# Performance work log

Hardware: AMD Instinct MI355X
Metric: run time of the kernel (lower is better)

Reference implementation:

```python
import math
import jax, jax.numpy as jnp
import numpy as np

DIM = 1024
DIM_HEAD = 64
NUM_HEAD = 16
HIDDEN = DIM_HEAD * NUM_HEAD  # 1024
B, L = 4, 2048
EPS = 1e-12  # torch F.normalize eps


def rms_norm(x, g):
    # F.normalize(x, dim=-1) * g * sqrt(d): L2-normalize then rescale
    d = x.shape[-1]
    norm = jnp.maximum(jnp.linalg.norm(x, axis=-1, keepdims=True), EPS)
    return x / norm * g * math.sqrt(d)


def setup_inputs() -> dict:
    key = jax.random.key(0)
    ks = jax.random.split(key, 8)
    x = jax.random.normal(ks[0], (B, L, DIM), dtype=jnp.float32)
    # torch Linear init scale ~ 1/sqrt(fan_in)
    s1 = 1.0 / math.sqrt(DIM)
    s2 = 1.0 / math.sqrt(HIDDEN)
    Wqkv = jax.random.uniform(ks[1], (3 * HIDDEN, DIM), minval=-s1, maxval=s1, dtype=jnp.float32)
    bqkv = jax.random.uniform(ks[2], (3 * HIDDEN,), minval=-s1, maxval=s1, dtype=jnp.float32)
    Wout = jax.random.uniform(ks[3], (DIM, HIDDEN), minval=-s2, maxval=s2, dtype=jnp.float32)
    bout = jax.random.uniform(ks[4], (DIM,), minval=-s2, maxval=s2, dtype=jnp.float32)
    g_q = jnp.ones((HIDDEN,), dtype=jnp.float32)
    g_k = jnp.ones((HIDDEN,), dtype=jnp.float32)
    g_out = jnp.ones((DIM,), dtype=jnp.float32)
    return {"x": x, "Wqkv": Wqkv, "bqkv": bqkv, "Wout": Wout, "bout": bout,
            "g_q": g_q, "g_k": g_k, "g_out": g_out}


def reference(x, Wqkv, bqkv, Wout, bout, g_q, g_k, g_out):
    scale = DIM_HEAD ** -0.5
    qkv = x @ Wqkv.T + bqkv  # (b, l, 3*hidden)
    q, k, v = jnp.split(qkv, 3, axis=-1)
    # QK RMSNorm applied over flattened (num_head*d) channel dim
    q = rms_norm(q, g_q)
    k = rms_norm(k, g_k)
    split_heads = lambda t: t.reshape(B, L, NUM_HEAD, DIM_HEAD).transpose(0, 2, 1, 3)
    q, k, v = split_heads(q), split_heads(k), split_heads(v)  # (b, h, l, d)
    q = q * scale
    sim = jnp.einsum('bhld,bhnd->bhln', q, k)
    attn = jax.nn.softmax(sim, axis=-1)
    out = jnp.einsum('bhln,bhnd->bhld', attn, v)  # (b, h, l, d)
    out = out.transpose(0, 2, 1, 3).reshape(B, L, HIDDEN)  # b l (h d)
    out = out @ Wout.T + bout
    return rms_norm(out, g_out)
```

## Files before the change

### kernel.cpp

```cpp
#include <hip/hip_runtime.h>
#include <math.h>

#define DIM       1024
#define DIM_HEAD  64
#define NUM_HEAD  16
#define HIDDEN    1024
#define BATCH     4
#define SEQ       2048
#define ROWS      (BATCH * SEQ)
#define QKV_N     (3 * HIDDEN)

typedef __bf16 bf16_t;
typedef __bf16 bf16x8 __attribute__((ext_vector_type(8)));
typedef __bf16 bf16x4 __attribute__((ext_vector_type(4)));
typedef float  f32x4  __attribute__((ext_vector_type(4)));

#define F32_ONE_PATTERN 0x3F800000u
#define LOG2E 1.44269504088896f

#define GLOAD_LDS16(gp, lp)                                                  \
    __builtin_amdgcn_global_load_lds(                                        \
        (const __attribute__((address_space(1))) void*)(const void*)(gp),    \
        (__attribute__((address_space(3))) void*)(void*)(lp), 16, 0, 0)

__global__ __launch_bounds__(256) void decode_bf16(const void* __restrict__ in,
                                                   bf16_t* __restrict__ out,
                                                   const unsigned* __restrict__ sniff,
                                                   long n)
{
    const bool isf32 = (*sniff == F32_ONE_PATTERN);
    const long i = ((long)blockIdx.x * 256 + threadIdx.x) * 8;
    if (i >= n) return;
    if (isf32) {
        const float* p = (const float*)in + i;
        f32x4 a = *(const f32x4*)p;
        f32x4 b = *(const f32x4*)(p + 4);
        bf16x8 r;
        r[0] = (bf16_t)a[0]; r[1] = (bf16_t)a[1]; r[2] = (bf16_t)a[2]; r[3] = (bf16_t)a[3];
        r[4] = (bf16_t)b[0]; r[5] = (bf16_t)b[1]; r[6] = (bf16_t)b[2]; r[7] = (bf16_t)b[3];
        *(bf16x8*)&out[i] = r;
    } else {
        *(bf16x8*)&out[i] = *(const bf16x8*)((const bf16_t*)in + i);
    }
}

__global__ __launch_bounds__(256) void decode_f32(const void* __restrict__ in,
                                                  float* __restrict__ out,
                                                  const unsigned* __restrict__ sniff,
                                                  long n)
{
    const bool isf32 = (*sniff == F32_ONE_PATTERN);
    const long i = ((long)blockIdx.x * 256 + threadIdx.x) * 8;
    if (i >= n) return;
    if (isf32) {
        const float* p = (const float*)in + i;
        *(f32x4*)&out[i]     = *(const f32x4*)p;
        *(f32x4*)&out[i + 4] = *(const f32x4*)(p + 4);
    } else {
        bf16x8 v = *(const bf16x8*)((const bf16_t*)in + i);
        f32x4 a, b;
        a[0] = (float)v[0]; a[1] = (float)v[1]; a[2] = (float)v[2]; a[3] = (float)v[3];
        b[0] = (float)v[4]; b[1] = (float)v[5]; b[2] = (float)v[6]; b[3] = (float)v[7];
        *(f32x4*)&out[i]     = a;
        *(f32x4*)&out[i + 4] = b;
    }
}

__global__ __launch_bounds__(256) void gemm_bt_bias(
    const bf16_t* __restrict__ A,
    const bf16_t* __restrict__ Bt,
    const float*  __restrict__ bias,
    bf16_t* __restrict__ C,
    int M, int N, int K)
{
    __shared__ __align__(16) bf16_t As[128 * 32];
    __shared__ __align__(16) bf16_t Bs[128 * 32];

    const int tid  = threadIdx.x;
    const int w    = tid >> 6;
    const int lane = tid & 63;
    const int wr   = w >> 1;
    const int wc   = w & 1;
    const int lr   = lane & 15;
    const int quad = lane >> 4;

    const int m0 = blockIdx.y * 128;
    const int n0 = blockIdx.x * 128;

    const int e0 = tid * 8;
    const int r0 = e0 >> 5;
    const int c0 = e0 & 31;
    const int r1 = r0 + 64;

    f32x4 acc[4][4];
    #pragma unroll
    for (int i = 0; i < 4; i++)
        #pragma unroll
        for (int j = 0; j < 4; j++)
            acc[i][j] = (f32x4){0.f, 0.f, 0.f, 0.f};

    const bf16_t* pa0 = &A [(size_t)(m0 + r0) * K + c0];
    const bf16_t* pa1 = &A [(size_t)(m0 + r1) * K + c0];
    const bf16_t* pb0 = &Bt[(size_t)(n0 + r0) * K + c0];
    const bf16_t* pb1 = &Bt[(size_t)(n0 + r1) * K + c0];

    for (int k0 = 0; k0 < K; k0 += 32) {
        __syncthreads();
        GLOAD_LDS16(pa0 + k0, &As[e0]);
        GLOAD_LDS16(pa1 + k0, &As[e0 + 2048]);
        GLOAD_LDS16(pb0 + k0, &Bs[e0]);
        GLOAD_LDS16(pb1 + k0, &Bs[e0 + 2048]);
        __syncthreads();

        bf16x8 af[4], bfr[4];
        #pragma unroll
        for (int i = 0; i < 4; i++)
            af[i] = *(const bf16x8*)&As[(wr * 64 + i * 16 + lr) * 32 + quad * 8];
        #pragma unroll
        for (int j = 0; j < 4; j++)
            bfr[j] = *(const bf16x8*)&Bs[(wc * 64 + j * 16 + lr) * 32 + quad * 8];
        #pragma unroll
        for (int i = 0; i < 4; i++)
            #pragma unroll
            for (int j = 0; j < 4; j++)
                acc[i][j] = __builtin_amdgcn_mfma_f32_16x16x32_bf16(
                    af[i], bfr[j], acc[i][j], 0, 0, 0);
    }

    #pragma unroll
    for (int i = 0; i < 4; i++) {
        const int row = m0 + wr * 64 + i * 16 + quad * 4;
        #pragma unroll
        for (int j = 0; j < 4; j++) {
            const int col = n0 + wc * 64 + j * 16 + lr;
            const float bv = bias[col];
            f32x4 v = acc[i][j];
            #pragma unroll
            for (int r = 0; r < 4; r++)
                C[(size_t)(row + r) * N + col] = (bf16_t)(v[r] + bv);
        }
    }
}

__device__ __forceinline__ void norm_apply(bf16_t* __restrict__ row,
                                           const float* __restrict__ g,
                                           float mult, int tid, float* red)
{
    bf16x4 xv = *(const bf16x4*)&row[tid * 4];
    float f0 = (float)xv[0], f1 = (float)xv[1], f2 = (float)xv[2], f3 = (float)xv[3];
    float ss = f0 * f0 + f1 * f1 + f2 * f2 + f3 * f3;
    #pragma unroll
    for (int off = 32; off > 0; off >>= 1) ss += __shfl_xor(ss, off, 64);
    if ((tid & 63) == 0) red[tid >> 6] = ss;
    __syncthreads();
    const float tot  = red[0] + red[1] + red[2] + red[3];
    const float fac  = mult / fmaxf(sqrtf(tot), 1e-12f);
    f32x4 gv = *(const f32x4*)&g[tid * 4];
    bf16x4 o;
    o[0] = (bf16_t)(f0 * gv[0] * fac);
    o[1] = (bf16_t)(f1 * gv[1] * fac);
    o[2] = (bf16_t)(f2 * gv[2] * fac);
    o[3] = (bf16_t)(f3 * gv[3] * fac);
    *(bf16x4*)&row[tid * 4] = o;
    __syncthreads();
}

__global__ __launch_bounds__(256) void qk_rmsnorm(bf16_t* __restrict__ qkv,
                                                  const float* __restrict__ gq,
                                                  const float* __restrict__ gk)
{
    __shared__ float red[4];
    const size_t base = (size_t)blockIdx.x * QKV_N;
    norm_apply(qkv + base, gq, 4.0f * LOG2E, threadIdx.x, red);
    norm_apply(qkv + base + HIDDEN, gk, 32.0f, threadIdx.x, red);
}

__global__ __launch_bounds__(256) void final_rmsnorm(const bf16_t* __restrict__ in,
                                                     const float* __restrict__ g,
                                                     void* __restrict__ out,
                                                     const unsigned* __restrict__ sniff)
{
    __shared__ float red[4];
    const bool isf32 = (*sniff == F32_ONE_PATTERN);
    const int tid = threadIdx.x;
    const bf16_t* row = in + (size_t)blockIdx.x * HIDDEN;

    bf16x4 xv = *(const bf16x4*)&row[tid * 4];
    float f0 = (float)xv[0], f1 = (float)xv[1], f2 = (float)xv[2], f3 = (float)xv[3];
    float ss = f0 * f0 + f1 * f1 + f2 * f2 + f3 * f3;
    #pragma unroll
    for (int off = 32; off > 0; off >>= 1) ss += __shfl_xor(ss, off, 64);
    if ((tid & 63) == 0) red[tid >> 6] = ss;
    __syncthreads();
    const float tot = red[0] + red[1] + red[2] + red[3];
    const float fac = 32.0f / fmaxf(sqrtf(tot), 1e-12f);
    f32x4 gv = *(const f32x4*)&g[tid * 4];
    f32x4 o;
    o[0] = f0 * gv[0] * fac;
    o[1] = f1 * gv[1] * fac;
    o[2] = f2 * gv[2] * fac;
    o[3] = f3 * gv[3] * fac;
    if (isf32) {
        *(f32x4*)((float*)out + (size_t)blockIdx.x * HIDDEN + tid * 4) = o;
    } else {
        bf16x4 ob;
        ob[0] = (bf16_t)o[0]; ob[1] = (bf16_t)o[1];
        ob[2] = (bf16_t)o[2]; ob[3] = (bf16_t)o[3];
        *(bf16x4*)((bf16_t*)out + (size_t)blockIdx.x * HIDDEN + tid * 4) = ob;
    }
}

__global__ __launch_bounds__(256) void transpose_v(const bf16_t* __restrict__ qkv,
                                                   bf16_t* __restrict__ vt)
{
    __shared__ bf16_t t[64][72];
    const int tid = threadIdx.x;
    const int bh = blockIdx.y, b = bh >> 4, h = bh & 15;
    const int l0 = blockIdx.x * 64;
    #pragma unroll
    for (int i = 0; i < 2; i++) {
        const int u = tid + i * 256;
        const int row = u >> 3, cg = u & 7;
        *(bf16x8*)&t[row][cg * 8] =
            *(const bf16x8*)&qkv[(size_t)(b * SEQ + l0 + row) * QKV_N + 2 * HIDDEN + h * 64 + cg * 8];
    }
    __syncthreads();
    #pragma unroll
    for (int i = 0; i < 2; i++) {
        const int u = tid + i * 256;
        const int d = u >> 3, lg = u & 7;
        bf16x8 o;
        #pragma unroll
        for (int e = 0; e < 8; e++) o[e] = t[lg * 8 + e][d];
        *(bf16x8*)&vt[((size_t)bh * 64 + d) * SEQ + l0 + lg * 8] = o;
    }
}

__global__ __launch_bounds__(256) void attn_mfma4(const bf16_t* __restrict__ qkv,
                                                  const bf16_t* __restrict__ vt,
                                                  bf16_t* __restrict__ out)
{
    __shared__ __align__(16) union {
        bf16_t Ps[4][64 * 40];
        float  Obuf[2][64][68];
    } sh;
    __shared__ float lred[4][4][16];

    const int tid  = threadIdx.x;
    const int w    = tid >> 6;
    const int lane = tid & 63;
    const int l15  = lane & 15;
    const int quad = lane >> 4;

    const int j    = blockIdx.x;
    const int xcd  = j & 7;
    const int slot = j >> 3;
    const int bh   = ((slot >> 5) << 3) | xcd;
    const int q0   = (slot & 31) * 64;
    const int b = bh >> 4, h = bh & 15;

    bf16x8 qf[4][2];
    #pragma unroll
    for (int qt = 0; qt < 4; qt++) {
        const bf16_t* qrow = qkv + (size_t)(b * SEQ + q0 + qt * 16 + l15) * QKV_N + h * DIM_HEAD;
        qf[qt][0] = *(const bf16x8*)&qrow[quad * 8];
        qf[qt][1] = *(const bf16x8*)&qrow[32 + quad * 8];
    }

    f32x4 O[4][4];
    float lp[4] = {0.f, 0.f, 0.f, 0.f};
    #pragma unroll
    for (int qt = 0; qt < 4; qt++)
        #pragma unroll
        for (int dt = 0; dt < 4; dt++)
            O[qt][dt] = (f32x4){0.f, 0.f, 0.f, 0.f};

    const bf16_t* kptr = qkv + (size_t)(b * SEQ + w * 32) * QKV_N + HIDDEN + h * DIM_HEAD;
    const bf16_t* vptr = vt + (size_t)bh * 64 * SEQ + w * 32;
    const int koff0 = l15 * QKV_N + quad * 8;
    const int koff1 = (16 + l15) * QKV_N + quad * 8;
    const int voff  = l15 * SEQ + quad * 8;
    bf16_t* const psw = sh.Ps[w] + l15 * 40 + quad * 4;
    const bf16_t* const psr = sh.Ps[w] + l15 * 40 + quad * 8;

    for (int it = 0; it < SEQ / 128; it++) {
        bf16x8 kA[2][2], vB[4];
        kA[0][0] = *(const bf16x8*)(kptr + koff0);
        kA[0][1] = *(const bf16x8*)(kptr + koff0 + 32);
        kA[1][0] = *(const bf16x8*)(kptr + koff1);
        kA[1][1] = *(const bf16x8*)(kptr + koff1 + 32);
        #pragma unroll
        for (int dt = 0; dt < 4; dt++)
            vB[dt] = *(const bf16x8*)(vptr + voff + dt * 16 * SEQ);
        kptr += 128 * QKV_N;
        vptr += 128;

        f32x4 s[2][4];
        #pragma unroll
        for (int kt = 0; kt < 2; kt++)
            #pragma unroll
            for (int qt = 0; qt < 4; qt++) {
                f32x4 z = (f32x4){0.f, 0.f, 0.f, 0.f};
                z = __builtin_amdgcn_mfma_f32_16x16x32_bf16(kA[kt][0], qf[qt][0], z, 0, 0, 0);
                s[kt][qt] = __builtin_amdgcn_mfma_f32_16x16x32_bf16(kA[kt][1], qf[qt][1], z, 0, 0, 0);
            }

        #pragma unroll
        for (int qt = 0; qt < 4; qt++)
            #pragma unroll
            for (int kt = 0; kt < 2; kt++) {
                bf16x4 pk;
                #pragma unroll
                for (int r = 0; r < 4; r++) {
                    const float p = __builtin_amdgcn_exp2f(s[kt][qt][r]);
                    lp[qt] += p;
                    pk[r] = (bf16_t)p;
                }
                *(bf16x4*)(psw + qt * 640 + kt * 16) = pk;
            }
        __builtin_amdgcn_s_waitcnt(0xC07F);

        #pragma unroll
        for (int qt = 0; qt < 4; qt++) {
            bf16x8 pf = *(const bf16x8*)(psr + qt * 640);
            #pragma unroll
            for (int dt = 0; dt < 4; dt++)
                O[qt][dt] = __builtin_amdgcn_mfma_f32_16x16x32_bf16(pf, vB[dt], O[qt][dt], 0, 0, 0);
        }
    }

    #pragma unroll
    for (int qt = 0; qt < 4; qt++) {
        lp[qt] += __shfl_xor(lp[qt], 16, 64);
        lp[qt] += __shfl_xor(lp[qt], 32, 64);
    }
    __syncthreads();
    if (w >= 2) {
        #pragma unroll
        for (int qt = 0; qt < 4; qt++)
            #pragma unroll
            for (int dt = 0; dt < 4; dt++)
                #pragma unroll
                for (int r = 0; r < 4; r++)
                    sh.Obuf[w - 2][qt * 16 + quad * 4 + r][dt * 16 + l15] = O[qt][dt][r];
    }
    if (quad == 0) {
        #pragma unroll
        for (int qt = 0; qt < 4; qt++) lred[w][qt][l15] = lp[qt];
    }
    __syncthreads();
    if (w < 2) {
        #pragma unroll
        for (int qt = 0; qt < 4; qt++)
            #pragma unroll
            for (int dt = 0; dt < 4; dt++)
                #pragma unroll
                for (int r = 0; r < 4; r++) {
                    float* p = &sh.Obuf[w][qt * 16 + quad * 4 + r][dt * 16 + l15];
                    *p += O[qt][dt][r];
                }
    }
    __syncthreads();
    #pragma unroll
    for (int i = 0; i < 2; i++) {
        const int u   = tid + i * 256;
        const int row = u >> 3;
        const int c8  = (u & 7) * 8;
        const float ls = lred[0][row >> 4][row & 15] + lred[1][row >> 4][row & 15]
                       + lred[2][row >> 4][row & 15] + lred[3][row >> 4][row & 15];
        const float inv = 1.0f / ls;
        f32x4 a0 = *(const f32x4*)&sh.Obuf[0][row][c8];
        f32x4 a1 = *(const f32x4*)&sh.Obuf[0][row][c8 + 4];
        f32x4 b0 = *(const f32x4*)&sh.Obuf[1][row][c8];
        f32x4 b1 = *(const f32x4*)&sh.Obuf[1][row][c8 + 4];
        bf16x8 o;
        o[0] = (bf16_t)((a0[0] + b0[0]) * inv);
        o[1] = (bf16_t)((a0[1] + b0[1]) * inv);
        o[2] = (bf16_t)((a0[2] + b0[2]) * inv);
        o[3] = (bf16_t)((a0[3] + b0[3]) * inv);
        o[4] = (bf16_t)((a1[0] + b1[0]) * inv);
        o[5] = (bf16_t)((a1[1] + b1[1]) * inv);
        o[6] = (bf16_t)((a1[2] + b1[2]) * inv);
        o[7] = (bf16_t)((a1[3] + b1[3]) * inv);
        *(bf16x8*)&out[(size_t)(b * SEQ + q0 + row) * HIDDEN + h * DIM_HEAD + c8] = o;
    }
}

extern "C" void kernel_launch(void* const* d_in, const int* in_sizes, int n_in,
                              void* d_out, int out_size, void* d_ws, size_t ws_size,
                              hipStream_t stream)
{
    (void)in_sizes; (void)n_in; (void)out_size; (void)ws_size;
    const void* x_raw    = d_in[0];
    const void* Wqkv_raw = d_in[1];
    const void* bqkv_raw = d_in[2];
    const void* Wout_raw = d_in[3];
    const void* bout_raw = d_in[4];
    const void* gq_raw   = d_in[5];
    const void* gk_raw   = d_in[6];
    const void* gout_raw = d_in[7];
    const unsigned* sniff = (const unsigned*)d_in[5];

    char* ws = (char*)d_ws;
    bf16_t* xb      = (bf16_t*)(ws + 0);
    bf16_t* Wqkvb   = (bf16_t*)(ws + (16l << 20));
    bf16_t* Woutb   = (bf16_t*)(ws + (22l << 20));
    float*  bqkv_f  = (float*) (ws + (24l << 20));
    float*  bout_f  = (float*) (ws + (24l << 20) + 16384);
    float*  gq_f    = (float*) (ws + (24l << 20) + 2 * 16384);
    float*  gk_f    = (float*) (ws + (24l << 20) + 3 * 16384);
    float*  gout_f  = (float*) (ws + (24l << 20) + 4 * 16384);
    bf16_t* qkv     = (bf16_t*)(ws + (25l << 20));
    bf16_t* vtb     = (bf16_t*)(ws + (73l << 20));
    bf16_t* attn_o  = xb;
    bf16_t* out_b   = qkv;

    decode_bf16<<<(ROWS * DIM) / 2048, 256, 0, stream>>>(x_raw, xb, sniff, (long)ROWS * DIM);
    decode_bf16<<<(QKV_N * DIM) / 2048, 256, 0, stream>>>(Wqkv_raw, Wqkvb, sniff, (long)QKV_N * DIM);
    decode_bf16<<<(DIM * HIDDEN) / 2048, 256, 0, stream>>>(Wout_raw, Woutb, sniff, (long)DIM * HIDDEN);
    decode_f32<<<2, 256, 0, stream>>>(bqkv_raw, bqkv_f, sniff, QKV_N);
    decode_f32<<<1, 256, 0, stream>>>(bout_raw, bout_f, sniff, DIM);
    decode_f32<<<1, 256, 0, stream>>>(gq_raw, gq_f, sniff, HIDDEN);
    decode_f32<<<1, 256, 0, stream>>>(gk_raw, gk_f, sniff, HIDDEN);
    decode_f32<<<1, 256, 0, stream>>>(gout_raw, gout_f, sniff, DIM);

    gemm_bt_bias<<<dim3(QKV_N / 128, ROWS / 128), 256, 0, stream>>>(
        xb, Wqkvb, bqkv_f, qkv, ROWS, QKV_N, DIM);
    qk_rmsnorm<<<ROWS, 256, 0, stream>>>(qkv, gq_f, gk_f);
    transpose_v<<<dim3(SEQ / 64, BATCH * NUM_HEAD), 256, 0, stream>>>(qkv, vtb);
    attn_mfma4<<<(SEQ / 64) * BATCH * NUM_HEAD, 256, 0, stream>>>(qkv, vtb, attn_o);
    gemm_bt_bias<<<dim3(HIDDEN / 128, ROWS / 128), 256, 0, stream>>>(
        attn_o, Woutb, bout_f, out_b, ROWS, HIDDEN, DIM);
    final_rmsnorm<<<ROWS, 256, 0, stream>>>(out_b, gout_f, d_out, sniff);
}
```

Baseline: 372.5 us.

## Halve attention query tile, compute row sums via MFMA, merge param decodes

The attention kernel now handles 32 query rows per block instead of 64, doubling the grid and cutting per-wave registers, with launch bounds requesting 4 blocks per CU. Softmax denominators are computed by an extra MFMA against a ones vector rather than scalar adds plus cross-lane shuffles, and the sums are stored in a spare shared-memory column. The five small parameter-decode launches are merged into one. The trade-off is that K/V tiles are reloaded twice as often per query and each iteration issues an extra MFMA.

Result: slower. 469.3 us (+26.0%).

```diff
diff --git a/kernel.cpp b/kernel.cpp
--- a/kernel.cpp
+++ b/kernel.cpp
@@ -44,25 +44,31 @@
     }
 }
 
-__global__ __launch_bounds__(256) void decode_f32(const void* __restrict__ in,
-                                                  float* __restrict__ out,
-                                                  const unsigned* __restrict__ sniff,
-                                                  long n)
+__global__ __launch_bounds__(256) void decode_params(
+    const void* __restrict__ bqkv_raw, const void* __restrict__ bout_raw,
+    const void* __restrict__ gq_raw,   const void* __restrict__ gk_raw,
+    const void* __restrict__ gout_raw,
+    float* __restrict__ o_bqkv, float* __restrict__ o_bout,
+    float* __restrict__ o_gq,   float* __restrict__ o_gk,
+    float* __restrict__ o_gout,
+    const unsigned* __restrict__ sniff)
 {
     const bool isf32 = (*sniff == F32_ONE_PATTERN);
-    const long i = ((long)blockIdx.x * 256 + threadIdx.x) * 8;
-    if (i >= n) return;
+    const int blk = blockIdx.x;
+    const void* src; float* dst; int off;
+    if (blk < 3)       { src = bqkv_raw; dst = o_bqkv; off = blk * 1024; }
+    else if (blk == 3) { src = bout_raw; dst = o_bout; off = 0; }
+    else if (blk == 4) { src = gq_raw;   dst = o_gq;   off = 0; }
+    else if (blk == 5) { src = gk_raw;   dst = o_gk;   off = 0; }
+    else               { src = gout_raw; dst = o_gout; off = 0; }
+    const int i = off + threadIdx.x * 4;
     if (isf32) {
-        const float* p = (const float*)in + i;
-        *(f32x4*)&out[i]     = *(const f32x4*)p;
-        *(f32x4*)&out[i + 4] = *(const f32x4*)(p + 4);
+        *(f32x4*)&dst[i] = *((const f32x4*)src + (off >> 2) + threadIdx.x);
     } else {
-        bf16x8 v = *(const bf16x8*)((const bf16_t*)in + i);
-        f32x4 a, b;
+        bf16x4 v = *((const bf16x4*)src + (off >> 2) + threadIdx.x);
+        f32x4 a;
         a[0] = (float)v[0]; a[1] = (float)v[1]; a[2] = (float)v[2]; a[3] = (float)v[3];
-        b[0] = (float)v[4]; b[1] = (float)v[5]; b[2] = (float)v[6]; b[3] = (float)v[7];
-        *(f32x4*)&out[i]     = a;
-        *(f32x4*)&out[i + 4] = b;
+        *(f32x4*)&dst[i] = a;
     }
 }
 
@@ -236,15 +242,14 @@
     }
 }
 
-__global__ __launch_bounds__(256) void attn_mfma4(const bf16_t* __restrict__ qkv,
-                                                  const bf16_t* __restrict__ vt,
-                                                  bf16_t* __restrict__ out)
+__global__ __launch_bounds__(256, 4) void attn_mfma5(const bf16_t* __restrict__ qkv,
+                                                     const bf16_t* __restrict__ vt,
+                                                     bf16_t* __restrict__ out)
 {
     __shared__ __align__(16) union {
-        bf16_t Ps[4][64 * 40];
-        float  Obuf[2][64][68];
+        bf16_t Ps[4][32 * 40];
+        float  Obuf[2][32][68];
     } sh;
-    __shared__ float lred[4][4][16];
 
     const int tid  = threadIdx.x;
     const int w    = tid >> 6;
@@ -255,25 +260,31 @@
     const int j    = blockIdx.x;
     const int xcd  = j & 7;
     const int slot = j >> 3;
-    const int bh   = ((slot >> 5) << 3) | xcd;
-    const int q0   = (slot & 31) * 64;
+    const int bh   = ((slot >> 6) << 3) | xcd;
+    const int q0   = (slot & 63) * 32;
     const int b = bh >> 4, h = bh & 15;
 
-    bf16x8 qf[4][2];
-    #pragma unroll
-    for (int qt = 0; qt < 4; qt++) {
+    bf16x8 qf[2][2];
+    #pragma unroll
+    for (int qt = 0; qt < 2; qt++) {
         const bf16_t* qrow = qkv + (size_t)(b * SEQ + q0 + qt * 16 + l15) * QKV_N + h * DIM_HEAD;
         qf[qt][0] = *(const bf16x8*)&qrow[quad * 8];
         qf[qt][1] = *(const bf16x8*)&qrow[32 + quad * 8];
     }
 
-    f32x4 O[4][4];
-    float lp[4] = {0.f, 0.f, 0.f, 0.f};
-    #pragma unroll
-    for (int qt = 0; qt < 4; qt++)
+    f32x4 O[2][4];
+    f32x4 ls[2];
+    #pragma unroll
+    for (int qt = 0; qt < 2; qt++) {
+        ls[qt] = (f32x4){0.f, 0.f, 0.f, 0.f};
         #pragma unroll
         for (int dt = 0; dt < 4; dt++)
             O[qt][dt] = (f32x4){0.f, 0.f, 0.f, 0.f};
+    }
+    bf16x8 vones;
+    #pragma unroll
+    for (int e = 0; e < 8; e++) vones[e] = (bf16_t)1.0f;
+    const f32x4 fzero = (f32x4){0.f, 0.f, 0.f, 0.f};
 
     const bf16_t* kptr = qkv + (size_t)(b * SEQ + w * 32) * QKV_N + HIDDEN + h * DIM_HEAD;
     const bf16_t* vptr = vt + (size_t)bh * 64 * SEQ + w * 32;
@@ -295,80 +306,73 @@
         kptr += 128 * QKV_N;
         vptr += 128;
 
-        f32x4 s[2][4];
+        f32x4 s[2][2];
         #pragma unroll
         for (int kt = 0; kt < 2; kt++)
             #pragma unroll
-            for (int qt = 0; qt < 4; qt++) {
-                f32x4 z = (f32x4){0.f, 0.f, 0.f, 0.f};
-                z = __builtin_amdgcn_mfma_f32_16x16x32_bf16(kA[kt][0], qf[qt][0], z, 0, 0, 0);
+            for (int qt = 0; qt < 2; qt++) {
+                f32x4 z = __builtin_amdgcn_mfma_f32_16x16x32_bf16(kA[kt][0], qf[qt][0], fzero, 0, 0, 0);
                 s[kt][qt] = __builtin_amdgcn_mfma_f32_16x16x32_bf16(kA[kt][1], qf[qt][1], z, 0, 0, 0);
             }
 
         #pragma unroll
-        for (int qt = 0; qt < 4; qt++)
+        for (int qt = 0; qt < 2; qt++)
             #pragma unroll
             for (int kt = 0; kt < 2; kt++) {
                 bf16x4 pk;
                 #pragma unroll
-                for (int r = 0; r < 4; r++) {
-                    const float p = __builtin_amdgcn_exp2f(s[kt][qt][r]);
-                    lp[qt] += p;
-                    pk[r] = (bf16_t)p;
-                }
+                for (int r = 0; r < 4; r++)
+                    pk[r] = (bf16_t)__builtin_amdgcn_exp2f(s[kt][qt][r]);
                 *(bf16x4*)(psw + qt * 640 + kt * 16) = pk;
             }
         __builtin_amdgcn_s_waitcnt(0xC07F);
 
         #pragma unroll
-        for (int qt = 0; qt < 4; qt++) {
+        for (int qt = 0; qt < 2; qt++) {
             bf16x8 pf = *(const bf16x8*)(psr + qt * 640);
+            ls[qt] = __builtin_amdgcn_mfma_f32_16x16x32_bf16(pf, vones, ls[qt], 0, 0, 0);
             #pragma unroll
             for (int dt = 0; dt < 4; dt++)
                 O[qt][dt] = __builtin_amdgcn_mfma_f32_16x16x32_bf16(pf, vB[dt], O[qt][dt], 0, 0, 0);
         }
     }
 
-    #pragma unroll
-    for (int qt = 0; qt < 4; qt++) {
-        lp[qt] += __shfl_xor(lp[qt], 16, 64);
-        lp[qt] += __shfl_xor(lp[qt], 32, 64);
-    }
     __syncthreads();
     if (w >= 2) {
         #pragma unroll
-        for (int qt = 0; qt < 4; qt++)
+        for (int qt = 0; qt < 2; qt++) {
             #pragma unroll
             for (int dt = 0; dt < 4; dt++)
                 #pragma unroll
                 for (int r = 0; r < 4; r++)
                     sh.Obuf[w - 2][qt * 16 + quad * 4 + r][dt * 16 + l15] = O[qt][dt][r];
-    }
-    if (quad == 0) {
-        #pragma unroll
-        for (int qt = 0; qt < 4; qt++) lred[w][qt][l15] = lp[qt];
+            if (l15 == 0)
+                #pragma unroll
+                for (int r = 0; r < 4; r++)
+                    sh.Obuf[w - 2][qt * 16 + quad * 4 + r][64] = ls[qt][r];
+        }
     }
     __syncthreads();
     if (w < 2) {
         #pragma unroll
-        for (int qt = 0; qt < 4; qt++)
+        for (int qt = 0; qt < 2; qt++) {
             #pragma unroll
             for (int dt = 0; dt < 4; dt++)
                 #pragma unroll
-                for (int r = 0; r < 4; r++) {
-                    float* p = &sh.Obuf[w][qt * 16 + quad * 4 + r][dt * 16 + l15];
-                    *p += O[qt][dt][r];
-                }
-    }
-    __syncthreads();
-    #pragma unroll
-    for (int i = 0; i < 2; i++) {
-        const int u   = tid + i * 256;
+                for (int r = 0; r < 4; r++)
+                    sh.Obuf[w][qt * 16 + quad * 4 + r][dt * 16 + l15] += O[qt][dt][r];
+            if (l15 == 0)
+                #pragma unroll
+                for (int r = 0; r < 4; r++)
+                    sh.Obuf[w][qt * 16 + quad * 4 + r][64] += ls[qt][r];
+        }
+    }
+    __syncthreads();
+    {
+        const int u   = tid;
         const int row = u >> 3;
         const int c8  = (u & 7) * 8;
-        const float ls = lred[0][row >> 4][row & 15] + lred[1][row >> 4][row & 15]
-                       + lred[2][row >> 4][row & 15] + lred[3][row >> 4][row & 15];
-        const float inv = 1.0f / ls;
+        const float inv = 1.0f / (sh.Obuf[0][row][64] + sh.Obuf[1][row][64]);
         f32x4 a0 = *(const f32x4*)&sh.Obuf[0][row][c8];
         f32x4 a1 = *(const f32x4*)&sh.Obuf[0][row][c8 + 4];
         f32x4 b0 = *(const f32x4*)&sh.Obuf[1][row][c8];
@@ -418,17 +422,14 @@
     decode_bf16<<<(ROWS * DIM) / 2048, 256, 0, stream>>>(x_raw, xb, sniff, (long)ROWS * DIM);
     decode_bf16<<<(QKV_N * DIM) / 2048, 256, 0, stream>>>(Wqkv_raw, Wqkvb, sniff, (long)QKV_N * DIM);
     decode_bf16<<<(DIM * HIDDEN) / 2048, 256, 0, stream>>>(Wout_raw, Woutb, sniff, (long)DIM * HIDDEN);
-    decode_f32<<<2, 256, 0, stream>>>(bqkv_raw, bqkv_f, sniff, QKV_N);
-    decode_f32<<<1, 256, 0, stream>>>(bout_raw, bout_f, sniff, DIM);
-    decode_f32<<<1, 256, 0, stream>>>(gq_raw, gq_f, sniff, HIDDEN);
-    decode_f32<<<1, 256, 0, stream>>>(gk_raw, gk_f, sniff, HIDDEN);
-    decode_f32<<<1, 256, 0, stream>>>(gout_raw, gout_f, sniff, DIM);
+    decode_params<<<7, 256, 0, stream>>>(bqkv_raw, bout_raw, gq_raw, gk_raw, gout_raw,
+                                         bqkv_f, bout_f, gq_f, gk_f, gout_f, sniff);
 
     gemm_bt_bias<<<dim3(QKV_N / 128, ROWS / 128), 256, 0, stream>>>(
         xb, Wqkvb, bqkv_f, qkv, ROWS, QKV_N, DIM);
     qk_rmsnorm<<<ROWS, 256, 0, stream>>>(qkv, gq_f, gk_f);
     transpose_v<<<dim3(SEQ / 64, BATCH * NUM_HEAD), 256, 0, stream>>>(qkv, vtb);
-    attn_mfma4<<<(SEQ / 64) * BATCH * NUM_HEAD, 256, 0, stream>>>(qkv, vtb, attn_o);
+    attn_mfma5<<<(SEQ / 32) * BATCH * NUM_HEAD, 256, 0, stream>>>(qkv, vtb, attn_o);
     gemm_bt_bias<<<dim3(HIDDEN / 128, ROWS / 128), 256, 0, stream>>>(
         attn_o, Woutb, bout_f, out_b, ROWS, HIDDEN, DIM);
     final_rmsnorm<<<ROWS, 256, 0, stream>>>(out_b, gout_f, d_out, sniff);
```

## Fuse V transpose into QKV GEMM epilogue and merge param decode launches

Applied to the files above, without the earlier changes.

The QKV GEMM is split so that Q/K columns go to a compact row-major buffer while V columns are written transposed straight into the per-head V^T layout. This removes the separate transpose_v kernel and its extra read and write of V. The five small parameter-decode launches are merged into one 7-block kernel to cut launch overhead. The transposed epilogue writes 4-element strided stores, which may coalesce worse than the old row-major store.

Result: faster. 356.4 us (-4.3%).

```diff
diff --git a/kernel.cpp b/kernel.cpp
--- a/kernel.cpp
+++ b/kernel.cpp
@@ -9,6 +9,7 @@
 #define SEQ       2048
 #define ROWS      (BATCH * SEQ)
 #define QKV_N     (3 * HIDDEN)
+#define QK_N      2048
 
 typedef __bf16 bf16_t;
 typedef __bf16 bf16x8 __attribute__((ext_vector_type(8)));
@@ -44,34 +45,40 @@
     }
 }
 
-__global__ __launch_bounds__(256) void decode_f32(const void* __restrict__ in,
-                                                  float* __restrict__ out,
-                                                  const unsigned* __restrict__ sniff,
-                                                  long n)
+__global__ __launch_bounds__(256) void decode_params(
+    const void* __restrict__ bqkv_raw, const void* __restrict__ bout_raw,
+    const void* __restrict__ gq_raw,   const void* __restrict__ gk_raw,
+    const void* __restrict__ gout_raw,
+    float* __restrict__ o_bqkv, float* __restrict__ o_bout,
+    float* __restrict__ o_gq,   float* __restrict__ o_gk,
+    float* __restrict__ o_gout,
+    const unsigned* __restrict__ sniff)
 {
     const bool isf32 = (*sniff == F32_ONE_PATTERN);
-    const long i = ((long)blockIdx.x * 256 + threadIdx.x) * 8;
-    if (i >= n) return;
+    const int blk = blockIdx.x;
+    const void* src; float* dst; int off;
+    if (blk < 3)       { src = bqkv_raw; dst = o_bqkv; off = blk * 1024; }
+    else if (blk == 3) { src = bout_raw; dst = o_bout; off = 0; }
+    else if (blk == 4) { src = gq_raw;   dst = o_gq;   off = 0; }
+    else if (blk == 5) { src = gk_raw;   dst = o_gk;   off = 0; }
+    else               { src = gout_raw; dst = o_gout; off = 0; }
+    const int i = off + threadIdx.x * 4;
     if (isf32) {
-        const float* p = (const float*)in + i;
-        *(f32x4*)&out[i]     = *(const f32x4*)p;
-        *(f32x4*)&out[i + 4] = *(const f32x4*)(p + 4);
+        *(f32x4*)&dst[i] = *((const f32x4*)src + (off >> 2) + threadIdx.x);
     } else {
-        bf16x8 v = *(const bf16x8*)((const bf16_t*)in + i);
-        f32x4 a, b;
+        bf16x4 v = *((const bf16x4*)src + (off >> 2) + threadIdx.x);
+        f32x4 a;
         a[0] = (float)v[0]; a[1] = (float)v[1]; a[2] = (float)v[2]; a[3] = (float)v[3];
-        b[0] = (float)v[4]; b[1] = (float)v[5]; b[2] = (float)v[6]; b[3] = (float)v[7];
-        *(f32x4*)&out[i]     = a;
-        *(f32x4*)&out[i + 4] = b;
-    }
-}
-
-__global__ __launch_bounds__(256) void gemm_bt_bias(
+        *(f32x4*)&dst[i] = a;
+    }
+}
+
+__global__ __launch_bounds__(256) void gemm_qkv(
     const bf16_t* __restrict__ A,
     const bf16_t* __restrict__ Bt,
     const float*  __restrict__ bias,
-    bf16_t* __restrict__ C,
-    int M, int N, int K)
+    bf16_t* __restrict__ qk,
+    bf16_t* __restrict__ vt)
 {
     __shared__ __align__(16) bf16_t As[128 * 32];
     __shared__ __align__(16) bf16_t Bs[128 * 32];
@@ -86,6 +93,106 @@
 
     const int m0 = blockIdx.y * 128;
     const int n0 = blockIdx.x * 128;
+    const int K  = DIM;
+
+    const int e0 = tid * 8;
+    const int r0 = e0 >> 5;
+    const int c0 = e0 & 31;
+    const int r1 = r0 + 64;
+
+    f32x4 acc[4][4];
+    #pragma unroll
+    for (int i = 0; i < 4; i++)
+        #pragma unroll
+        for (int j = 0; j < 4; j++)
+            acc[i][j] = (f32x4){0.f, 0.f, 0.f, 0.f};
+
+    const bf16_t* pa0 = &A [(size_t)(m0 + r0) * K + c0];
+    const bf16_t* pa1 = &A [(size_t)(m0 + r1) * K + c0];
+    const bf16_t* pb0 = &Bt[(size_t)(n0 + r0) * K + c0];
+    const bf16_t* pb1 = &Bt[(size_t)(n0 + r1) * K + c0];
+
+    for (int k0 = 0; k0 < K; k0 += 32) {
+        __syncthreads();
+        GLOAD_LDS16(pa0 + k0, &As[e0]);
+        GLOAD_LDS16(pa1 + k0, &As[e0 + 2048]);
+        GLOAD_LDS16(pb0 + k0, &Bs[e0]);
+        GLOAD_LDS16(pb1 + k0, &Bs[e0 + 2048]);
+        __syncthreads();
+
+        bf16x8 af[4], bfr[4];
+        #pragma unroll
+        for (int i = 0; i < 4; i++)
+            af[i] = *(const bf16x8*)&As[(wr * 64 + i * 16 + lr) * 32 + quad * 8];
+        #pragma unroll
+        for (int j = 0; j < 4; j++)
+            bfr[j] = *(const bf16x8*)&Bs[(wc * 64 + j * 16 + lr) * 32 + quad * 8];
+        #pragma unroll
+        for (int i = 0; i < 4; i++)
+            #pragma unroll
+            for (int j = 0; j < 4; j++)
+                acc[i][j] = __builtin_amdgcn_mfma_f32_16x16x32_bf16(
+                    af[i], bfr[j], acc[i][j], 0, 0, 0);
+    }
+
+    if (n0 < 2048) {
+        #pragma unroll
+        for (int i = 0; i < 4; i++) {
+            const int row = m0 + wr * 64 + i * 16 + quad * 4;
+            #pragma unroll
+            for (int j = 0; j < 4; j++) {
+                const int col = n0 + wc * 64 + j * 16 + lr;
+                const float bv = bias[col];
+                f32x4 v = acc[i][j];
+                #pragma unroll
+                for (int r = 0; r < 4; r++)
+                    qk[(size_t)(row + r) * QK_N + col] = (bf16_t)(v[r] + bv);
+            }
+        }
+    } else {
+        const int b  = m0 >> 11;
+        const int l0 = (m0 & 2047) + wr * 64 + quad * 4;
+        #pragma unroll
+        for (int j = 0; j < 4; j++) {
+            const int c = (n0 - 2048) + wc * 64 + j * 16 + lr;
+            const int h = c >> 6, d = c & 63;
+            const float bv = bias[2048 + c];
+            bf16_t* vrow = vt + ((size_t)((b << 4) | h) * 64 + d) * SEQ;
+            #pragma unroll
+            for (int i = 0; i < 4; i++) {
+                f32x4 v = acc[i][j];
+                bf16x4 o;
+                o[0] = (bf16_t)(v[0] + bv);
+                o[1] = (bf16_t)(v[1] + bv);
+                o[2] = (bf16_t)(v[2] + bv);
+                o[3] = (bf16_t)(v[3] + bv);
+                *(bf16x4*)&vrow[l0 + i * 16] = o;
+            }
+        }
+    }
+}
+
+__global__ __launch_bounds__(256) void gemm_out(
+    const bf16_t* __restrict__ A,
+    const bf16_t* __restrict__ Bt,
+    const float*  __restrict__ bias,
+    bf16_t* __restrict__ C)
+{
+    __shared__ __align__(16) bf16_t As[128 * 32];
+    __shared__ __align__(16) bf16_t Bs[128 * 32];
+
+    const int tid  = threadIdx.x;
+    const int w    = tid >> 6;
+    const int lane = tid & 63;
+    const int wr   = w >> 1;
+    const int wc   = w & 1;
+    const int lr   = lane & 15;
+    const int quad = lane >> 4;
+
+    const int m0 = blockIdx.y * 128;
+    const int n0 = blockIdx.x * 128;
+    const int K  = HIDDEN;
+    const int N  = DIM;
 
     const int e0 = tid * 8;
     const int r0 = e0 >> 5;
@@ -165,14 +272,14 @@
     __syncthreads();
 }
 
-__global__ __launch_bounds__(256) void qk_rmsnorm(bf16_t* __restrict__ qkv,
+__global__ __launch_bounds__(256) void qk_rmsnorm(bf16_t* __restrict__ qk,
                                                   const float* __restrict__ gq,
                                                   const float* __restrict__ gk)
 {
     __shared__ float red[4];
-    const size_t base = (size_t)blockIdx.x * QKV_N;
-    norm_apply(qkv + base, gq, 4.0f * LOG2E, threadIdx.x, red);
-    norm_apply(qkv + base + HIDDEN, gk, 32.0f, threadIdx.x, red);
+    const size_t base = (size_t)blockIdx.x * QK_N;
+    norm_apply(qk + base, gq, 4.0f * LOG2E, threadIdx.x, red);
+    norm_apply(qk + base + HIDDEN, gk, 32.0f, threadIdx.x, red);
 }
 
 __global__ __launch_bounds__(256) void final_rmsnorm(const bf16_t* __restrict__ in,
@@ -210,33 +317,7 @@
     }
 }
 
-__global__ __launch_bounds__(256) void transpose_v(const bf16_t* __restrict__ qkv,
-                                                   bf16_t* __restrict__ vt)
-{
-    __shared__ bf16_t t[64][72];
-    const int tid = threadIdx.x;
-    const int bh = blockIdx.y, b = bh >> 4, h = bh & 15;
-    const int l0 = blockIdx.x * 64;
-    #pragma unroll
-    for (int i = 0; i < 2; i++) {
-        const int u = tid + i * 256;
-        const int row = u >> 3, cg = u & 7;
-        *(bf16x8*)&t[row][cg * 8] =
-            *(const bf16x8*)&qkv[(size_t)(b * SEQ + l0 + row) * QKV_N + 2 * HIDDEN + h * 64 + cg * 8];
-    }
-    __syncthreads();
-    #pragma unroll
-    for (int i = 0; i < 2; i++) {
-        const int u = tid + i * 256;
-        const int d = u >> 3, lg = u & 7;
-        bf16x8 o;
-        #pragma unroll
-        for (int e = 0; e < 8; e++) o[e] = t[lg * 8 + e][d];
-        *(bf16x8*)&vt[((size_t)bh * 64 + d) * SEQ + l0 + lg * 8] = o;
-    }
-}
-
-__global__ __launch_bounds__(256) void attn_mfma4(const bf16_t* __restrict__ qkv,
+__global__ __launch_bounds__(256) void attn_mfma7(const bf16_t* __restrict__ qk,
                                                   const bf16_t* __restrict__ vt,
                                                   bf16_t* __restrict__ out)
 {
@@ -262,7 +343,7 @@
     bf16x8 qf[4][2];
     #pragma unroll
     for (int qt = 0; qt < 4; qt++) {
-        const bf16_t* qrow = qkv + (size_t)(b * SEQ + q0 + qt * 16 + l15) * QKV_N + h * DIM_HEAD;
+        const bf16_t* qrow = qk + (size_t)(b * SEQ + q0 + qt * 16 + l15) * QK_N + h * DIM_HEAD;
         qf[qt][0] = *(const bf16x8*)&qrow[quad * 8];
         qf[qt][1] = *(const bf16x8*)&qrow[32 + quad * 8];
     }
@@ -275,10 +356,10 @@
         for (int dt = 0; dt < 4; dt++)
             O[qt][dt] = (f32x4){0.f, 0.f, 0.f, 0.f};
 
-    const bf16_t* kptr = qkv + (size_t)(b * SEQ + w * 32) * QKV_N + HIDDEN + h * DIM_HEAD;
+    const bf16_t* kptr = qk + (size_t)(b * SEQ + w * 32) * QK_N + HIDDEN + h * DIM_HEAD;
     const bf16_t* vptr = vt + (size_t)bh * 64 * SEQ + w * 32;
-    const int koff0 = l15 * QKV_N + quad * 8;
-    const int koff1 = (16 + l15) * QKV_N + quad * 8;
+    const int koff0 = l15 * QK_N + quad * 8;
+    const int koff1 = (16 + l15) * QK_N + quad * 8;
     const int voff  = l15 * SEQ + quad * 8;
     bf16_t* const psw = sh.Ps[w] + l15 * 40 + quad * 4;
     const bf16_t* const psr = sh.Ps[w] + l15 * 40 + quad * 8;
@@ -292,7 +373,7 @@
         #pragma unroll
         for (int dt = 0; dt < 4; dt++)
             vB[dt] = *(const bf16x8*)(vptr + voff + dt * 16 * SEQ);
-        kptr += 128 * QKV_N;
+        kptr += 128 * QK_N;
         vptr += 128;
 
         f32x4 s[2][4];
@@ -410,26 +491,22 @@
     float*  gq_f    = (float*) (ws + (24l << 20) + 2 * 16384);
     float*  gk_f    = (float*) (ws + (24l << 20) + 3 * 16384);
     float*  gout_f  = (float*) (ws + (24l << 20) + 4 * 16384);
-    bf16_t* qkv     = (bf16_t*)(ws + (25l << 20));
-    bf16_t* vtb     = (bf16_t*)(ws + (73l << 20));
+    bf16_t* qk      = (bf16_t*)(ws + (25l << 20));
+    bf16_t* vtb     = (bf16_t*)(ws + (57l << 20));
     bf16_t* attn_o  = xb;
-    bf16_t* out_b   = qkv;
+    bf16_t* out_b   = qk;
 
     decode_bf16<<<(ROWS * DIM) / 2048, 256, 0, stream>>>(x_raw, xb, sniff, (long)ROWS * DIM);
     decode_bf16<<<(QKV_N * DIM) / 2048, 256, 0, stream>>>(Wqkv_raw, Wqkvb, sniff, (long)QKV_N * DIM);
     decode_bf16<<<(DIM * HIDDEN) / 2048, 256, 0, stream>>>(Wout_raw, Woutb, sniff, (long)DIM * HIDDEN);
-    decode_f32<<<2, 256, 0, stream>>>(bqkv_raw, bqkv_f, sniff, QKV_N);
-    decode_f32<<<1, 256, 0, stream>>>(bout_raw, bout_f, sniff, DIM);
-    decode_f32<<<1, 256, 0, stream>>>(gq_raw, gq_f, sniff, HIDDEN);
-    decode_f32<<<1, 256, 0, stream>>>(gk_raw, gk_f, sniff, HIDDEN);
-    decode_f32<<<1, 256, 0, stream>>>(gout_raw, gout_f, sniff, DIM);
-
-    gemm_bt_bias<<<dim3(QKV_N / 128, ROWS / 128), 256, 0, stream>>>(
-        xb, Wqkvb, bqkv_f, qkv, ROWS, QKV_N, DIM);
-    qk_rmsnorm<<<ROWS, 256, 0, stream>>>(qkv, gq_f, gk_f);
-    transpose_v<<<dim3(SEQ / 64, BATCH * NUM_HEAD), 256, 0, stream>>>(qkv, vtb);
-    attn_mfma4<<<(SEQ / 64) * BATCH * NUM_HEAD, 256, 0, stream>>>(qkv, vtb, attn_o);
-    gemm_bt_bias<<<dim3(HIDDEN / 128, ROWS / 128), 256, 0, stream>>>(
-        attn_o, Woutb, bout_f, out_b, ROWS, HIDDEN, DIM);
+    decode_params<<<7, 256, 0, stream>>>(bqkv_raw, bout_raw, gq_raw, gk_raw, gout_raw,
+                                         bqkv_f, bout_f, gq_f, gk_f, gout_f, sniff);
+
+    gemm_qkv<<<dim3(QKV_N / 128, ROWS / 128), 256, 0, stream>>>(
+        xb, Wqkvb, bqkv_f, qk, vtb);
+    qk_rmsnorm<<<ROWS, 256, 0, stream>>>(qk, gq_f, gk_f);
+    attn_mfma7<<<(SEQ / 64) * BATCH * NUM_HEAD, 256, 0, stream>>>(qk, vtb, attn_o);
+    gemm_out<<<dim3(DIM / 128, ROWS / 128), 256, 0, stream>>>(
+        attn_o, Woutb, bout_f, out_b);
     final_rmsnorm<<<ROWS, 256, 0, stream>>>(out_b, gout_f, d_out, sniff);
 }
```
